# Performance work log

Measured on AMD Instinct MI355X. Metric: run time of the kernel, lower is better.

Reference implementation:

```python
import jax, jax.numpy as jnp
import numpy as np

N_GRAPHS = 20000
N_NODES = 7          # nodes per NAS cell
HID = 256            # hidden_dim
N_OPS = 5
TAU = 1.0


def _glorot(key, shape):
    s = 1.0 / np.sqrt(shape[0])
    return jax.random.normal(key, shape, jnp.float32) * s


def setup_inputs() -> dict:
    key = jax.random.key(0)
    ks = jax.random.split(key, 12)
    N = N_GRAPHS * N_NODES
    # fully-connected DAG edges inside each graph (upper triangular, 21 per graph)
    sl, dl = np.triu_indices(N_NODES, k=1)
    offs = (np.arange(N_GRAPHS) * N_NODES)[:, None]
    src = (offs + sl[None, :]).reshape(-1)
    dst = (offs + dl[None, :]).reshape(-1)
    edge_index = jnp.asarray(np.stack([src, dst]), dtype=jnp.int32)  # [2, E]
    batch = jnp.asarray(np.repeat(np.arange(N_GRAPHS), N_NODES), dtype=jnp.int32)
    E = edge_index.shape[1]
    return {
        "x": jax.random.normal(ks[0], (N, HID), jnp.float32),
        "edge_index": edge_index,
        "batch": batch,
        "W1": _glorot(ks[1], (HID, HID)), "b1": jnp.zeros((HID,), jnp.float32),
        "W2": _glorot(ks[2], (HID, HID)), "b2": jnp.zeros((HID,), jnp.float32),
        "We": _glorot(ks[3], (2 * HID, 2)), "be": jnp.zeros((2,), jnp.float32),
        "Wm": _glorot(ks[4], (HID, N_OPS)), "bm": jnp.zeros((N_OPS,), jnp.float32),
        "g_edge": jax.random.gumbel(ks[5], (E, 2), jnp.float32),
        "g_op": jax.random.gumbel(ks[6], (N, N_OPS), jnp.float32),
    }


def gcn_conv(x, edge_index, W, b, edge_weight=None):
    """PyG-style GCNConv: add self-loops (weight 1), symmetric normalization."""
    N = x.shape[0]
    src, dst = edge_index[0], edge_index[1]
    E = src.shape[0]
    ew = jnp.ones((E,), x.dtype) if edge_weight is None else edge_weight
    loop = jnp.arange(N, dtype=src.dtype)
    src_a = jnp.concatenate([src, loop])
    dst_a = jnp.concatenate([dst, loop])
    ew_a = jnp.concatenate([ew, jnp.ones((N,), x.dtype)])
    deg = jax.ops.segment_sum(ew_a, dst_a, num_segments=N)
    dinv = jnp.where(deg > 0, jax.lax.rsqrt(jnp.maximum(deg, 1e-12)), 0.0)
    norm = dinv[src_a] * ew_a * dinv[dst_a]  # [E+N]
    h = x @ W  # [N, out]
    msg = norm[:, None] * h[src_a]
    return jax.ops.segment_sum(msg, dst_a, num_segments=N) + b


def gumbel_softmax(logits, g, tau, hard):
    y = jax.nn.softmax((logits + g) / tau, axis=-1)
    if hard:
        y_hard = jax.nn.one_hot(jnp.argmax(y, axis=-1), y.shape[-1], dtype=y.dtype)
        y = y_hard + y - jax.lax.stop_gradient(y)
    return y


def reference(x, edge_index, batch, W1, b1, W2, b2, We, be, Wm, bm, g_edge, g_op):
    # mu=2 GCN layers with ReLU
    h = jax.nn.relu(gcn_conv(x, edge_index, W1, b1))
    h = jax.nn.relu(gcn_conv(h, edge_index, W2, b2))
    # edge scorer: 2-way gumbel-softmax over (keep, drop) per edge
    src, dst = edge_index[0], edge_index[1]
    pair = jnp.concatenate([h[src], h[dst]], axis=-1)  # [E, 2*HID]
    edge_logits = pair @ We + be                       # [E, 2]
    edges_scores = gumbel_softmax(edge_logits, g_edge, TAU, hard=False)
    # sample_pre=False branch: average the two score channels as edge weight
    avg_scores = (edges_scores[:, 0] + edges_scores[:, 1]) / 2
    op_emb = gcn_conv(h, edge_index, Wm, bm, edge_weight=avg_scores)  # [N, N_OPS]
    # hard straight-through gumbel-softmax over operations
    op_indices = gumbel_softmax(op_emb, g_op, TAU, hard=True)
    return op_indices
```

## Files before the change

### kernel.cpp

```cpp
#include <hip/hip_runtime.h>
#include <math.h>

#define HID 256

typedef __attribute__((ext_vector_type(8))) short v8s;
typedef __attribute__((ext_vector_type(4))) float v4f;

__device__ __forceinline__ float d1c(int i){ return 1.0f/sqrtf((float)(i+1)); }
__device__ __forceinline__ float d2c(int i){ return 1.0f/sqrtf(1.0f+0.5f*(float)i); }

__device__ __forceinline__ unsigned short f2bf(float x){
    unsigned u = __float_as_uint(x);
    u += 0x7fffu + ((u>>16)&1u);
    return (unsigned short)(u>>16);
}
__device__ __forceinline__ float bf2f(unsigned short b){
    return __uint_as_float(((unsigned)b)<<16);
}

__device__ __forceinline__ void mixA1_4(float (&v)[7][4]) {
#pragma unroll
    for (int r = 6; r >= 0; --r) {
        float t[4] = {0, 0, 0, 0};
#pragma unroll
        for (int i = 0; i <= r; ++i) {
            const float c = d1c(i) * d1c(r);
#pragma unroll
            for (int j = 0; j < 4; ++j) t[j] = fmaf(c, v[i][j], t[j]);
        }
#pragma unroll
        for (int j = 0; j < 4; ++j) v[r][j] = t[j];
    }
}

__global__ void prep_w(const float* __restrict__ W1, const float* __restrict__ W2,
                       unsigned short* __restrict__ outw)
{
    const int tid = blockIdx.x*256 + threadIdx.x;
    if (tid >= 2*3*8*16*64) return;
    const int l  = tid & 63;
    const int c  = tid >> 6;
    const int nt = c & 15;
    const int k0 = (c>>4) & 7;
    const int s  = (c>>7) % 3;
    const int L  = c / (3*8*16);
    const float* W = L ? W2 : W1;
    const int n = nt*16 + (l & 15);
    unsigned short* o = outw + (size_t)tid*8;
#pragma unroll
    for (int e = 0; e < 8; ++e){
        const int k = k0*32 + (l>>4)*8 + e;
        float x = W[k*HID + n];
        unsigned short b0 = f2bf(x); float rr = x - bf2f(b0);
        unsigned short b1 = f2bf(rr); rr -= bf2f(b1);
        unsigned short b2 = f2bf(rr);
        o[e] = (s==0)? b0 : (s==1)? b1 : b2;
    }
}

__global__ __launch_bounds__(256, 2)
void nas_mfma(const float* __restrict__ X,
              const float* __restrict__ b1, const float* __restrict__ b2,
              const float* __restrict__ Wm, const float* __restrict__ bm,
              const float* __restrict__ g_op,
              const unsigned short* __restrict__ Bw,
              float* __restrict__ out)
{
    __shared__ __align__(16) char smem[49152 + 16384];
    char* sb = smem;
    float* bnc = (float*)(smem + 49152);

    const int t   = threadIdx.x;
    const int w   = t >> 6;
    const int l   = t & 63;
    const int l15 = l & 15;
    const int q   = l >> 4;
    const int g   = t >> 5;
    const int t31 = t & 31;
    const long node0 = (long)blockIdx.x * 56;

    auto writeSplits = [&](float (&v)[7][4]){
        const int kl   = 4*t31;
        const int hs   = kl >> 3;
        const int sub8 = (kl & 7) * 2;
#pragma unroll
        for (int r = 0; r < 7; ++r){
            const int row  = g*7 + r;
            const int slot = hs ^ (row & 7);
            char* p = sb + row*256 + slot*16 + sub8;
            unsigned short h0[4], h1[4], h2[4];
#pragma unroll
            for (int j = 0; j < 4; ++j){
                float x = v[r][j];
                h0[j] = f2bf(x); float rr = x - bf2f(h0[j]);
                h1[j] = f2bf(rr); rr -= bf2f(h1[j]);
                h2[j] = f2bf(rr);
            }
            *(uint2*)(p)         = make_uint2((unsigned)h0[0]|((unsigned)h0[1]<<16),
                                              (unsigned)h0[2]|((unsigned)h0[3]<<16));
            *(uint2*)(p+16384)   = make_uint2((unsigned)h1[0]|((unsigned)h1[1]<<16),
                                              (unsigned)h1[2]|((unsigned)h1[3]<<16));
            *(uint2*)(p+32768)   = make_uint2((unsigned)h2[0]|((unsigned)h2[1]<<16),
                                              (unsigned)h2[2]|((unsigned)h2[3]<<16));
        }
    };

    auto gemm_half = [&](v4f (&ac)[4][4], const unsigned short* lbase, int h){
#pragma unroll 1
        for (int ks = 0; ks < 4; ++ks){
            const int ksg = h*4 + ks;
            v8s A[3][4];
            const int xorslot = ((ks*4 + q) ^ (l & 7)) << 4;
#pragma unroll
            for (int s = 0; s < 3; ++s)
#pragma unroll
            for (int mt = 0; mt < 4; ++mt)
                A[s][mt] = *(const v8s*)(sb + s*16384 + (mt*16 + l15)*256 + xorslot);
#pragma unroll 1
            for (int s2 = 0; s2 < 3; ++s2){
                const unsigned short* bp = lbase + (size_t)(((s2*8 + ksg)*16) + w)*512
                                                 + (size_t)l*8;
                v8s B0 = *(const v8s*)(bp);
                v8s B1 = *(const v8s*)(bp + 2048);
                v8s B2 = *(const v8s*)(bp + 4096);
                v8s B3 = *(const v8s*)(bp + 6144);
#pragma unroll
                for (int mt = 0; mt < 4; ++mt){
                    ac[mt][0] = __builtin_amdgcn_mfma_f32_16x16x32_bf16(A[0][mt], B0, ac[mt][0],0,0,0);
                    ac[mt][1] = __builtin_amdgcn_mfma_f32_16x16x32_bf16(A[0][mt], B1, ac[mt][1],0,0,0);
                    ac[mt][2] = __builtin_amdgcn_mfma_f32_16x16x32_bf16(A[0][mt], B2, ac[mt][2],0,0,0);
                    ac[mt][3] = __builtin_amdgcn_mfma_f32_16x16x32_bf16(A[0][mt], B3, ac[mt][3],0,0,0);
                }
                if (s2 < 2){
#pragma unroll
                    for (int mt = 0; mt < 4; ++mt){
                        ac[mt][0] = __builtin_amdgcn_mfma_f32_16x16x32_bf16(A[1][mt], B0, ac[mt][0],0,0,0);
                        ac[mt][1] = __builtin_amdgcn_mfma_f32_16x16x32_bf16(A[1][mt], B1, ac[mt][1],0,0,0);
                        ac[mt][2] = __builtin_amdgcn_mfma_f32_16x16x32_bf16(A[1][mt], B2, ac[mt][2],0,0,0);
                        ac[mt][3] = __builtin_amdgcn_mfma_f32_16x16x32_bf16(A[1][mt], B3, ac[mt][3],0,0,0);
                    }
                }
                if (s2 == 0){
#pragma unroll
                    for (int mt = 0; mt < 4; ++mt){
                        ac[mt][0] = __builtin_amdgcn_mfma_f32_16x16x32_bf16(A[2][mt], B0, ac[mt][0],0,0,0);
                        ac[mt][1] = __builtin_amdgcn_mfma_f32_16x16x32_bf16(A[2][mt], B1, ac[mt][1],0,0,0);
                        ac[mt][2] = __builtin_amdgcn_mfma_f32_16x16x32_bf16(A[2][mt], B2, ac[mt][2],0,0,0);
                        ac[mt][3] = __builtin_amdgcn_mfma_f32_16x16x32_bf16(A[2][mt], B3, ac[mt][3],0,0,0);
                    }
                }
            }
        }
    };

    auto bounceWrite = [&](v4f (&ac)[4][4], int p){
        const int colp = (w*16 + l15) ^ ((q & 1) << 4);
#pragma unroll
        for (int mt = 0; mt < 4; ++mt)
#pragma unroll
        for (int j = 0; j < 4; ++j)
            bnc[(mt*16 + q*4 + j)*64 + colp] = ac[mt][p][j];
    };
    auto bounceRead = [&](float (&v)[7][4]){
        const int cl = 4*(t31 & 15);
#pragma unroll
        for (int r = 0; r < 7; ++r){
            const int row = g*7 + r;
            const int sw  = ((row >> 2) & 1) << 4;
            float4 f = *(const float4*)(&bnc[row*64 + (cl ^ sw)]);
            v[r][0]=f.x; v[r][1]=f.y; v[r][2]=f.z; v[r][3]=f.w;
        }
    };

    v4f acc[4][4];
#pragma unroll
    for (int mt=0;mt<4;++mt)
#pragma unroll
    for (int p=0;p<4;++p) acc[mt][p] = (v4f){0.f,0.f,0.f,0.f};

#pragma unroll
    for (int h = 0; h < 2; ++h){
        {
            float v[7][4];
            const float* xp = X + (node0 + g*7)*HID + h*128 + 4*t31;
#pragma unroll
            for (int r = 0; r < 7; ++r){
                float4 f = *(const float4*)(xp + (long)r*HID);
                v[r][0]=f.x; v[r][1]=f.y; v[r][2]=f.z; v[r][3]=f.w;
            }
            mixA1_4(v);
            writeSplits(v);
        }
        __syncthreads();
        gemm_half(acc, Bw, h);
        __syncthreads();
    }

    v4f acc2[4][4];
#pragma unroll
    for (int mt=0;mt<4;++mt)
#pragma unroll
    for (int p=0;p<4;++p) acc2[mt][p] = (v4f){0.f,0.f,0.f,0.f};

#pragma unroll
    for (int h = 0; h < 2; ++h){
#pragma unroll
        for (int sub = 0; sub < 2; ++sub){
            bounceWrite(acc, 2*h + sub);
            __syncthreads();
            if ((t31 >> 4) == sub){
                float v[7][4];
                bounceRead(v);
                const int colg = h*128 + 4*t31;
                float4 bb = *(const float4*)(b1 + colg);
                const float bia[4] = {bb.x, bb.y, bb.z, bb.w};
#pragma unroll
                for (int r = 0; r < 7; ++r)
#pragma unroll
                for (int j = 0; j < 4; ++j)
                    v[r][j] = fmaxf(v[r][j] + bia[j], 0.0f);
                mixA1_4(v);
                writeSplits(v);
            }
            __syncthreads();
        }
        gemm_half(acc2, Bw + 196608, h);
        __syncthreads();
    }

    float pm[7][5];
#pragma unroll
    for (int r=0;r<7;++r)
#pragma unroll
    for (int p=0;p<5;++p) pm[r][p] = 0.0f;

#pragma unroll
    for (int h = 0; h < 2; ++h)
#pragma unroll
    for (int sub = 0; sub < 2; ++sub){
        bounceWrite(acc2, 2*h + sub);
        __syncthreads();
        if ((t31 >> 4) == sub){
            float v[7][4];
            bounceRead(v);
            const int colg = h*128 + 4*t31;
            float4 bb = *(const float4*)(b2 + colg);
            const float bia[4] = {bb.x, bb.y, bb.z, bb.w};
#pragma unroll
            for (int r = 0; r < 7; ++r)
#pragma unroll
            for (int j = 0; j < 4; ++j)
                v[r][j] = fmaxf(v[r][j] + bia[j], 0.0f);
#pragma unroll
            for (int j = 0; j < 4; ++j){
                const float* wr = Wm + (colg + j)*5;
                float w5[5];
#pragma unroll
                for (int p = 0; p < 5; ++p) w5[p] = wr[p];
#pragma unroll
                for (int r = 0; r < 7; ++r)
#pragma unroll
                for (int p = 0; p < 5; ++p)
                    pm[r][p] = fmaf(v[r][j], w5[p], pm[r][p]);
            }
        }
        __syncthreads();
    }

#pragma unroll
    for (int m = 16; m >= 1; m >>= 1)
#pragma unroll
        for (int r = 0; r < 7; ++r)
#pragma unroll
            for (int p = 0; p < 5; ++p)
                pm[r][p] += __shfl_xor(pm[r][p], m, 64);

    if (t31 < 7){
        const int rr = t31;
        const long node = node0 + g*7 + rr;
        const float d2r = d2c(rr);
        float op[5];
#pragma unroll
        for (int p = 0; p < 5; ++p) op[p] = bm[p];
#pragma unroll
        for (int i = 0; i < 7; ++i){
            const float wgt = (i > rr) ? 0.0f
                            : (((i < rr) ? 0.5f : 1.0f) * d2c(i) * d2r);
#pragma unroll
            for (int p = 0; p < 5; ++p)
                op[p] = fmaf(wgt, pm[i][p], op[p]);
        }
        const float* gp = g_op + node*5;
        float best = op[0] + gp[0];
        int bi = 0;
#pragma unroll
        for (int p = 1; p < 5; ++p){
            float u = op[p] + gp[p];
            if (u > best) { best = u; bi = p; }
        }
        float* o = out + node*5;
#pragma unroll
        for (int p = 0; p < 5; ++p) o[p] = (p == bi) ? 1.0f : 0.0f;
    }
}

extern "C" void kernel_launch(void* const* d_in, const int* in_sizes, int n_in,
                              void* d_out, int out_size, void* d_ws, size_t ws_size,
                              hipStream_t stream)
{
    const float* X   = (const float*)d_in[0];
    const float* W1  = (const float*)d_in[3];
    const float* b1  = (const float*)d_in[4];
    const float* W2  = (const float*)d_in[5];
    const float* b2  = (const float*)d_in[6];
    const float* Wm  = (const float*)d_in[9];
    const float* bm  = (const float*)d_in[10];
    const float* gop = (const float*)d_in[12];
    float* out = (float*)d_out;

    unsigned short* wsplit = (unsigned short*)d_ws;

    prep_w<<<192, 256, 0, stream>>>(W1, W2, wsplit);

    const int N       = in_sizes[0] / HID;
    const int ngraph  = N / 7;
    const int nblocks = ngraph / 8;

    nas_mfma<<<nblocks, 256, 0, stream>>>(X, b1, b2, Wm, bm, gop, wsplit, out);
}
```

Baseline: 441.2 us.

## Software-pipeline B loads in GEMM and widen bounce buffer to cut barriers

Flattens the GEMM inner loops into a fully unrolled 12-step sequence with triple-buffered B-fragment prefetch two steps ahead. It also doubles the LDS bounce buffer so a full half of columns is staged at once, with a new swizzle, instead of four quarter passes. The input half-tile and the second layer-1 half are loaded or computed early in registers and overlap with the GEMM. This cuts syncthreads and idle threads per stage and hides global B-load latency. The cost is higher LDS use (80KB per block, which may threaten 2 blocks per CU) and more register pressure from the prefetch buffers and vh1.

```diff
diff --git a/kernel.cpp b/kernel.cpp
--- a/kernel.cpp
+++ b/kernel.cpp
@@ -66,8 +66,8 @@
               const unsigned short* __restrict__ Bw,
               float* __restrict__ out)
 {
-    __shared__ __align__(16) char smem[49152 + 16384];
-    char* sb = smem;
+    __shared__ __align__(16) char smem[49152 + 32768];
+    char*  sb  = smem;
     float* bnc = (float*)(smem + 49152);
 
     const int t   = threadIdx.x;
@@ -79,7 +79,7 @@
     const int t31 = t & 31;
     const long node0 = (long)blockIdx.x * 56;
 
-    auto writeSplits = [&](float (&v)[7][4]){
+    auto writeSplits = [&](const float (&v)[7][4]){
         const int kl   = 4*t31;
         const int hs   = kl >> 3;
         const int sub8 = (kl & 7) * 2;
@@ -106,71 +106,82 @@
     };
 
     auto gemm_half = [&](v4f (&ac)[4][4], const unsigned short* lbase, int h){
-#pragma unroll 1
-        for (int ks = 0; ks < 4; ++ks){
-            const int ksg = h*4 + ks;
-            v8s A[3][4];
-            const int xorslot = ((ks*4 + q) ^ (l & 7)) << 4;
-#pragma unroll
-            for (int s = 0; s < 3; ++s)
-#pragma unroll
-            for (int mt = 0; mt < 4; ++mt)
-                A[s][mt] = *(const v8s*)(sb + s*16384 + (mt*16 + l15)*256 + xorslot);
-#pragma unroll 1
-            for (int s2 = 0; s2 < 3; ++s2){
-                const unsigned short* bp = lbase + (size_t)(((s2*8 + ksg)*16) + w)*512
-                                                 + (size_t)l*8;
-                v8s B0 = *(const v8s*)(bp);
-                v8s B1 = *(const v8s*)(bp + 2048);
-                v8s B2 = *(const v8s*)(bp + 4096);
-                v8s B3 = *(const v8s*)(bp + 6144);
+        const unsigned short* bbase = lbase + (size_t)w*512 + (size_t)l*8;
+        v8s Bb[3][4];
+        v8s A[3][4];
+        auto loadB = [&](int gi, int buf){
+            const int ks = gi / 3, s2 = gi % 3;
+            const unsigned short* bp = bbase + (size_t)((s2*8 + h*4 + ks)*16)*512;
+            Bb[buf][0] = *(const v8s*)(bp);
+            Bb[buf][1] = *(const v8s*)(bp + 2048);
+            Bb[buf][2] = *(const v8s*)(bp + 4096);
+            Bb[buf][3] = *(const v8s*)(bp + 6144);
+        };
+        loadB(0, 0);
+        loadB(1, 1);
+#pragma unroll
+        for (int gi = 0; gi < 12; ++gi){
+            const int ks = gi / 3, s2 = gi % 3;
+            if (s2 == 0){
+                const int xorslot = ((ks*4 + q) ^ (l & 7)) << 4;
+#pragma unroll
+                for (int s = 0; s < 3; ++s)
+#pragma unroll
+                for (int mt = 0; mt < 4; ++mt)
+                    A[s][mt] = *(const v8s*)(sb + s*16384 + (mt*16 + l15)*256 + xorslot);
+            }
+            if (gi + 2 < 12) loadB(gi + 2, (gi + 2) % 3);
+            const int buf = gi % 3;
+#pragma unroll
+            for (int s1 = 0; s1 < 3; ++s1){
+                if (s1 + s2 > 2) continue;
 #pragma unroll
                 for (int mt = 0; mt < 4; ++mt){
-                    ac[mt][0] = __builtin_amdgcn_mfma_f32_16x16x32_bf16(A[0][mt], B0, ac[mt][0],0,0,0);
-                    ac[mt][1] = __builtin_amdgcn_mfma_f32_16x16x32_bf16(A[0][mt], B1, ac[mt][1],0,0,0);
-                    ac[mt][2] = __builtin_amdgcn_mfma_f32_16x16x32_bf16(A[0][mt], B2, ac[mt][2],0,0,0);
-                    ac[mt][3] = __builtin_amdgcn_mfma_f32_16x16x32_bf16(A[0][mt], B3, ac[mt][3],0,0,0);
-                }
-                if (s2 < 2){
-#pragma unroll
-                    for (int mt = 0; mt < 4; ++mt){
-                        ac[mt][0] = __builtin_amdgcn_mfma_f32_16x16x32_bf16(A[1][mt], B0, ac[mt][0],0,0,0);
-                        ac[mt][1] = __builtin_amdgcn_mfma_f32_16x16x32_bf16(A[1][mt], B1, ac[mt][1],0,0,0);
-                        ac[mt][2] = __builtin_amdgcn_mfma_f32_16x16x32_bf16(A[1][mt], B2, ac[mt][2],0,0,0);
-                        ac[mt][3] = __builtin_amdgcn_mfma_f32_16x16x32_bf16(A[1][mt], B3, ac[mt][3],0,0,0);
-                    }
-                }
-                if (s2 == 0){
-#pragma unroll
-                    for (int mt = 0; mt < 4; ++mt){
-                        ac[mt][0] = __builtin_amdgcn_mfma_f32_16x16x32_bf16(A[2][mt], B0, ac[mt][0],0,0,0);
-                        ac[mt][1] = __builtin_amdgcn_mfma_f32_16x16x32_bf16(A[2][mt], B1, ac[mt][1],0,0,0);
-                        ac[mt][2] = __builtin_amdgcn_mfma_f32_16x16x32_bf16(A[2][mt], B2, ac[mt][2],0,0,0);
-                        ac[mt][3] = __builtin_amdgcn_mfma_f32_16x16x32_bf16(A[2][mt], B3, ac[mt][3],0,0,0);
-                    }
+                    ac[mt][0] = __builtin_amdgcn_mfma_f32_16x16x32_bf16(A[s1][mt], Bb[buf][0], ac[mt][0],0,0,0);
+                    ac[mt][1] = __builtin_amdgcn_mfma_f32_16x16x32_bf16(A[s1][mt], Bb[buf][1], ac[mt][1],0,0,0);
+                    ac[mt][2] = __builtin_amdgcn_mfma_f32_16x16x32_bf16(A[s1][mt], Bb[buf][2], ac[mt][2],0,0,0);
+                    ac[mt][3] = __builtin_amdgcn_mfma_f32_16x16x32_bf16(A[s1][mt], Bb[buf][3], ac[mt][3],0,0,0);
                 }
             }
         }
     };
 
-    auto bounceWrite = [&](v4f (&ac)[4][4], int p){
-        const int colp = (w*16 + l15) ^ ((q & 1) << 4);
-#pragma unroll
-        for (int mt = 0; mt < 4; ++mt)
-#pragma unroll
-        for (int j = 0; j < 4; ++j)
-            bnc[(mt*16 + q*4 + j)*64 + colp] = ac[mt][p][j];
-    };
-    auto bounceRead = [&](float (&v)[7][4]){
-        const int cl = 4*(t31 & 15);
+    auto bw2 = [&](const v4f (&ac)[4][4], int h){
+#pragma unroll
+        for (int pb = 0; pb < 2; ++pb){
+            const int p  = 2*h + pb;
+            const int lc = (w + 4*pb)*16 + l15;
+#pragma unroll
+            for (int mt = 0; mt < 4; ++mt){
+                const int sw = ((q&1)<<4) ^ ((q>>1)<<2);
+#pragma unroll
+                for (int j = 0; j < 4; ++j){
+                    const int row = mt*16 + q*4 + j;
+                    bnc[row*128 + (lc ^ sw)] = ac[mt][p][j];
+                }
+            }
+        }
+    };
+    auto br2 = [&](float (&v)[7][4]){
+        const int lc = 4*t31;
 #pragma unroll
         for (int r = 0; r < 7; ++r){
             const int row = g*7 + r;
-            const int sw  = ((row >> 2) & 1) << 4;
-            float4 f = *(const float4*)(&bnc[row*64 + (cl ^ sw)]);
+            const int qq  = (row>>2)&3;
+            const int sw  = ((qq&1)<<4) ^ ((qq>>1)<<2);
+            float4 f = *(const float4*)(&bnc[row*128 + (lc ^ sw)]);
             v[r][0]=f.x; v[r][1]=f.y; v[r][2]=f.z; v[r][3]=f.w;
         }
     };
+    auto biasRelu = [&](float (&v)[7][4], const float* bias, int h){
+        float4 bb = *(const float4*)(bias + h*128 + 4*t31);
+        const float bia[4] = {bb.x, bb.y, bb.z, bb.w};
+#pragma unroll
+        for (int r = 0; r < 7; ++r)
+#pragma unroll
+        for (int j = 0; j < 4; ++j)
+            v[r][j] = fmaxf(v[r][j] + bia[j], 0.0f);
+    };
 
     v4f acc[4][4];
 #pragma unroll
@@ -178,23 +189,27 @@
 #pragma unroll
     for (int p=0;p<4;++p) acc[mt][p] = (v4f){0.f,0.f,0.f,0.f};
 
-#pragma unroll
-    for (int h = 0; h < 2; ++h){
-        {
-            float v[7][4];
-            const float* xp = X + (node0 + g*7)*HID + h*128 + 4*t31;
-#pragma unroll
-            for (int r = 0; r < 7; ++r){
-                float4 f = *(const float4*)(xp + (long)r*HID);
-                v[r][0]=f.x; v[r][1]=f.y; v[r][2]=f.z; v[r][3]=f.w;
-            }
-            mixA1_4(v);
-            writeSplits(v);
-        }
-        __syncthreads();
-        gemm_half(acc, Bw, h);
-        __syncthreads();
-    }
+    float vh1[7][4];
+    {
+        float v0[7][4];
+        const float* xp = X + (node0 + g*7)*HID + 4*t31;
+#pragma unroll
+        for (int r = 0; r < 7; ++r){
+            float4 f0 = *(const float4*)(xp + (long)r*HID);
+            float4 f1 = *(const float4*)(xp + (long)r*HID + 128);
+            v0[r][0]=f0.x; v0[r][1]=f0.y; v0[r][2]=f0.z; v0[r][3]=f0.w;
+            vh1[r][0]=f1.x; vh1[r][1]=f1.y; vh1[r][2]=f1.z; vh1[r][3]=f1.w;
+        }
+        mixA1_4(v0);
+        mixA1_4(vh1);
+        writeSplits(v0);
+    }
+    __syncthreads();
+    gemm_half(acc, Bw, 0);
+    __syncthreads();
+    writeSplits(vh1);
+    __syncthreads();
+    gemm_half(acc, Bw, 1);
 
     v4f acc2[4][4];
 #pragma unroll
@@ -202,31 +217,27 @@
 #pragma unroll
     for (int p=0;p<4;++p) acc2[mt][p] = (v4f){0.f,0.f,0.f,0.f};
 
-#pragma unroll
-    for (int h = 0; h < 2; ++h){
-#pragma unroll
-        for (int sub = 0; sub < 2; ++sub){
-            bounceWrite(acc, 2*h + sub);
-            __syncthreads();
-            if ((t31 >> 4) == sub){
-                float v[7][4];
-                bounceRead(v);
-                const int colg = h*128 + 4*t31;
-                float4 bb = *(const float4*)(b1 + colg);
-                const float bia[4] = {bb.x, bb.y, bb.z, bb.w};
-#pragma unroll
-                for (int r = 0; r < 7; ++r)
-#pragma unroll
-                for (int j = 0; j < 4; ++j)
-                    v[r][j] = fmaxf(v[r][j] + bia[j], 0.0f);
-                mixA1_4(v);
-                writeSplits(v);
-            }
-            __syncthreads();
-        }
-        gemm_half(acc2, Bw + 196608, h);
-        __syncthreads();
-    }
+    __syncthreads();
+    bw2(acc, 0);
+    __syncthreads();
+    {
+        float v[7][4];
+        br2(v);
+        biasRelu(v, b1, 0);
+        mixA1_4(v);
+        writeSplits(v);
+    }
+    __syncthreads();
+    bw2(acc, 1);
+    __syncthreads();
+    br2(vh1);
+    biasRelu(vh1, b1, 1);
+    mixA1_4(vh1);
+    gemm_half(acc2, Bw + 196608, 0);
+    __syncthreads();
+    writeSplits(vh1);
+    __syncthreads();
+    gemm_half(acc2, Bw + 196608, 1);
 
     float pm[7][5];
 #pragma unroll
@@ -234,38 +245,33 @@
 #pragma unroll
     for (int p=0;p<5;++p) pm[r][p] = 0.0f;
 
-#pragma unroll
-    for (int h = 0; h < 2; ++h)
-#pragma unroll
-    for (int sub = 0; sub < 2; ++sub){
-        bounceWrite(acc2, 2*h + sub);
-        __syncthreads();
-        if ((t31 >> 4) == sub){
-            float v[7][4];
-            bounceRead(v);
-            const int colg = h*128 + 4*t31;
-            float4 bb = *(const float4*)(b2 + colg);
-            const float bia[4] = {bb.x, bb.y, bb.z, bb.w};
+    auto stage_pm = [&](int h){
+        float v[7][4];
+        br2(v);
+        biasRelu(v, b2, h);
+        const int colg = h*128 + 4*t31;
+#pragma unroll
+        for (int j = 0; j < 4; ++j){
+            const float* wr = Wm + (colg + j)*5;
+            float w5[5];
+#pragma unroll
+            for (int p = 0; p < 5; ++p) w5[p] = wr[p];
 #pragma unroll
             for (int r = 0; r < 7; ++r)
 #pragma unroll
-            for (int j = 0; j < 4; ++j)
-                v[r][j] = fmaxf(v[r][j] + bia[j], 0.0f);
-#pragma unroll
-            for (int j = 0; j < 4; ++j){
-                const float* wr = Wm + (colg + j)*5;
-                float w5[5];
-#pragma unroll
-                for (int p = 0; p < 5; ++p) w5[p] = wr[p];
-#pragma unroll
-                for (int r = 0; r < 7; ++r)
-#pragma unroll
-                for (int p = 0; p < 5; ++p)
-                    pm[r][p] = fmaf(v[r][j], w5[p], pm[r][p]);
-            }
-        }
-        __syncthreads();
-    }
+            for (int p = 0; p < 5; ++p)
+                pm[r][p] = fmaf(v[r][j], w5[p], pm[r][p]);
+        }
+    };
+
+    __syncthreads();
+    bw2(acc2, 0);
+    __syncthreads();
+    stage_pm(0);
+    __syncthreads();
+    bw2(acc2, 1);
+    __syncthreads();
+    stage_pm(1);
 
 #pragma unroll
     for (int m = 16; m >= 1; m >>= 1)
```

Measured after the change: 400.6 us. 1.1x faster.
